# Optimization experiments

Hardware: AMD Instinct MI355X
Metric: run time of the kernel (lower is better)

The kernel has to match this reference:

```python
import jax, jax.numpy as jnp
import numpy as np
import math

B, T, S = 8, 8, 64
L = T * S            # 512 tokens per modality
D = 1024             # bi_hidden_size
H = 16               # bi_num_attention_heads
DH = D // H          # 64 head size (queries)
DKV = D // 2         # 512 kv projection size
SCALE = 1.0 / math.sqrt(DH)


def setup_inputs() -> dict:
    key = jax.random.key(0)
    ks = jax.random.split(key, 24)
    inp = {
        "input_tensor1": jax.random.normal(ks[0], (B, T, S, D), jnp.float32),
        "attention_mask1": jnp.zeros((B, 1, 1, L), jnp.float32),
        "input_tensor2": jax.random.normal(ks[1], (B, T, S, D), jnp.float32),
        "attention_mask2": jnp.zeros((B, 1, 1, L), jnp.float32),
        "input_tensor3": jax.random.normal(ks[2], (B, T, S, D), jnp.float32),
        "attention_mask3": jnp.zeros((B, 1, 1, L), jnp.float32),
    }
    # Linear params, stored as [in, out]; y = x @ W + b
    kidx = 3
    for i in (1, 2, 3):
        inp[f"w_q{i}"] = jax.random.normal(ks[kidx], (D, D), jnp.float32) * 0.02; kidx += 1
        inp[f"b_q{i}"] = jnp.zeros((D,), jnp.float32)
        inp[f"w_k{i}"] = jax.random.normal(ks[kidx], (D, DKV), jnp.float32) * 0.02; kidx += 1
        inp[f"b_k{i}"] = jnp.zeros((DKV,), jnp.float32)
        inp[f"w_v{i}"] = jax.random.normal(ks[kidx], (D, DKV), jnp.float32) * 0.02; kidx += 1
        inp[f"b_v{i}"] = jnp.zeros((DKV,), jnp.float32)
    return inp


def _heads(x):
    # [B, L, H*dh] -> [B, H, L, dh]
    b, l, d = x.shape
    return x.reshape(b, l, H, d // H).transpose(0, 2, 1, 3)


def _branch(q, k_a, k_b, v_a, v_b, bias):
    # keys/values concatenated along the per-head feature dim (dim 3)
    k = jnp.concatenate([k_a, k_b], axis=-1)          # [B,H,L,dh]
    v = jnp.concatenate([v_a, v_b], axis=-1)          # [B,H,L,dh]
    scores = jnp.einsum('bhqd,bhkd->bhqk', q, k) * SCALE + bias
    probs = jax.nn.softmax(scores, axis=-1)           # [B,H,L,L]
    ctx = jnp.einsum('bhqk,bhkd->bhqd', probs, v)     # [B,H,L,dh]
    ctx = ctx.transpose(0, 2, 1, 3).reshape(q.shape[0], T, S, D)
    return ctx, probs


def reference(input_tensor1, attention_mask1, input_tensor2, attention_mask2,
              input_tensor3, attention_mask3,
              w_q1, b_q1, w_k1, b_k1, w_v1, b_v1,
              w_q2, b_q2, w_k2, b_k2, w_v2, b_v2,
              w_q3, b_q3, w_k3, b_k3, w_v3, b_v3):
    b = input_tensor1.shape[0]
    x1 = input_tensor1.reshape(b, L, -1)
    x2 = input_tensor2.reshape(b, L, -1)
    x3 = input_tensor3.reshape(b, L, -1)
    m1 = attention_mask1.reshape(b, 1, 1, L)
    m2 = attention_mask2.reshape(b, 1, 1, L)
    m3 = attention_mask3.reshape(b, 1, 1, L)

    q1 = _heads(x1 @ w_q1 + b_q1); k1 = _heads(x1 @ w_k1 + b_k1); v1 = _heads(x1 @ w_v1 + b_v1)
    q2 = _heads(x2 @ w_q2 + b_q2); k2 = _heads(x2 @ w_k2 + b_k2); v2 = _heads(x2 @ w_v2 + b_v2)
    q3 = _heads(x3 @ w_q3 + b_q3); k3 = _heads(x3 @ w_k3 + b_k3); v3 = _heads(x3 @ w_v3 + b_v3)

    # branch 1: Q from modality2, KV from 1+3, mask bias from masks 1&3
    c1, p1 = _branch(q2, k1, k3, v1, v3, m1 + m3)
    # branch 2: Q from modality1, KV from 2+3, no mask bias
    c2, p2 = _branch(q1, k2, k3, v2, v3, jnp.zeros((), jnp.float32))
    # branch 3: Q from modality3, KV from 1+2, mask bias from masks 1&2
    c3, p3 = _branch(q3, k1, k2, v1, v2, m1 + m2)

    return (c2, c1, c3, (p2, p1, p3))
```

## Files before the change

### kernel.cpp

```cpp
#include <hip/hip_runtime.h>
#include <hip/hip_bf16.h>

typedef __bf16 bf16x8 __attribute__((ext_vector_type(8)));
typedef float f32x4 __attribute__((ext_vector_type(4)));

#define ATT_SCALE 0.125f

static __device__ __forceinline__ unsigned short f2bf(float f){
  unsigned u = __float_as_uint(f);
  u += 0x7fffu + ((u >> 16) & 1u);
  return (unsigned short)(u >> 16);
}
static __device__ __forceinline__ bf16x8 ld_bf8(const unsigned short* p){
  uint4 u = *(const uint4*)p;
  return __builtin_bit_cast(bf16x8, u);
}
static __device__ __forceinline__ f32x4 mfma16(bf16x8 a, bf16x8 b, f32x4 c){
  return __builtin_amdgcn_mfma_f32_16x16x32_bf16(a, b, c, 0, 0, 0);
}
static __device__ __forceinline__ void gload16(const unsigned short* g, unsigned short* l){
  __builtin_amdgcn_global_load_lds(
      (const __attribute__((address_space(1))) unsigned*)g,
      (__attribute__((address_space(3))) unsigned*)l, 16, 0, 0);
}
static __device__ __forceinline__ void lgkm_bar(){
  asm volatile("s_waitcnt lgkmcnt(0)" ::: "memory");
  __builtin_amdgcn_s_barrier();
  __builtin_amdgcn_sched_barrier(0);
}

struct WtArgs { const float* src[9]; unsigned short* dst[9]; int N[9]; };
__global__ void wtrans(WtArgs a){
  int z = blockIdx.z;
  int N = a.N[z];
  int n0 = blockIdx.x*32;
  if(n0 >= N) return;
  int k0 = blockIdx.y*32;
  const float* W = a.src[z];
  unsigned short* WT = a.dst[z];
  __shared__ float t[32][33];
  int tx = threadIdx.x, ty = threadIdx.y;
  #pragma unroll
  for(int r=0;r<4;++r){
    int row = ty + r*8;
    t[row][tx] = W[(size_t)(k0+row)*N + n0+tx];
  }
  __syncthreads();
  #pragma unroll
  for(int r=0;r<4;++r){
    int row = ty + r*8;
    WT[(size_t)(n0+row)*1024 + k0+tx] = f2bf(t[tx][row]);
  }
}

struct GemmArgs {
  const float* X[3]; const unsigned short* WT[3];
  const float* bq[3]; const float* bk[3]; const float* bv[3];
  unsigned short* C[3];
};
__global__ __launch_bounds__(256) void gemm_qkv(GemmArgs g){
  __shared__ unsigned short As[128*32];
  __shared__ unsigned short Bs[128*32];
  int z = blockIdx.z;
  const float* A = g.X[z];
  const unsigned short* Bt = g.WT[z];
  unsigned short* C = g.C[z];
  int tid = threadIdx.x;
  int wave = tid>>6, lane = tid&63, l15 = lane&15, l4 = lane>>4;
  int m0 = blockIdx.y*128, n0 = blockIdx.x*128;
  int wr = wave>>1, wc = wave&1;
  f32x4 acc[4][4];
  #pragma unroll
  for(int i=0;i<4;++i)
    #pragma unroll
    for(int j=0;j<4;++j) acc[i][j] = (f32x4){0.f,0.f,0.f,0.f};

  int c0r = tid,      row0 = c0r>>2, col0 = (c0r&3)*8;
  int c1r = tid+256,  row1 = c1r>>2, col1 = (c1r&3)*8;
  const float* a0p = A + (size_t)(m0+row0)*1024 + col0;
  const float* a1p = A + (size_t)(m0+row1)*1024 + col1;
  const unsigned short* b0p = Bt + (size_t)(n0+row0)*1024 + col0;
  const unsigned short* b1p = Bt + (size_t)(n0+row1)*1024 + col1;

  for(int k0=0; k0<1024; k0+=32){
    gload16(b0p + k0, &Bs[c0r*8]);
    gload16(b1p + k0, &Bs[c1r*8]);
    float4 fa0 = *(const float4*)(a0p + k0);
    float4 fa1 = *(const float4*)(a0p + k0 + 4);
    float4 fb0 = *(const float4*)(a1p + k0);
    float4 fb1 = *(const float4*)(a1p + k0 + 4);
    ushort4 u0 = {f2bf(fa0.x), f2bf(fa0.y), f2bf(fa0.z), f2bf(fa0.w)};
    ushort4 u1 = {f2bf(fa1.x), f2bf(fa1.y), f2bf(fa1.z), f2bf(fa1.w)};
    ushort4 u2 = {f2bf(fb0.x), f2bf(fb0.y), f2bf(fb0.z), f2bf(fb0.w)};
    ushort4 u3 = {f2bf(fb1.x), f2bf(fb1.y), f2bf(fb1.z), f2bf(fb1.w)};
    *(ushort4*)&As[c0r*8]     = u0;
    *(ushort4*)&As[c0r*8 + 4] = u1;
    *(ushort4*)&As[c1r*8]     = u2;
    *(ushort4*)&As[c1r*8 + 4] = u3;
    __syncthreads();
    bf16x8 af[4], bfr[4];
    #pragma unroll
    for(int t=0;t<4;++t){
      af[t]  = ld_bf8(&As[(wr*64 + t*16 + l15)*32 + 8*l4]);
      bfr[t] = ld_bf8(&Bs[(wc*64 + t*16 + l15)*32 + 8*l4]);
    }
    #pragma unroll
    for(int mt=0;mt<4;++mt)
      #pragma unroll
      for(int nt=0;nt<4;++nt)
        acc[mt][nt] = mfma16(af[mt], bfr[nt], acc[mt][nt]);
    __syncthreads();
  }

  #pragma unroll
  for(int mt=0;mt<4;++mt){
    #pragma unroll
    for(int nt=0;nt<4;++nt){
      int col = n0 + wc*64 + nt*16 + l15;
      float bb;
      if(col < 1024)      bb = g.bq[z][col];
      else if(col < 1536) bb = g.bk[z][col-1024];
      else                bb = g.bv[z][col-1536];
      #pragma unroll
      for(int r=0;r<4;++r){
        int row = m0 + wr*64 + mt*16 + l4*4 + r;
        C[(size_t)row*2048 + col] = f2bf(acc[mt][nt][r] + bb);
      }
    }
  }
}

struct VtArgs { const unsigned short* in[3]; unsigned short* out[3]; };
__global__ __launch_bounds__(256) void vtrans(VtArgs a){
  int z = blockIdx.z;
  const unsigned short* in = a.in[z];
  unsigned short* out = a.out[z];
  __shared__ unsigned short T[64][72];
  int r0 = blockIdx.x*64, c0 = blockIdx.y*64;
  int tid = threadIdx.x;
  #pragma unroll
  for(int p=0;p<4;++p){
    int e = p*1024 + tid*4;
    int row = e>>6, col = e&63;
    *(ushort4*)&T[row][col] = *(const ushort4*)&in[(size_t)(r0+row)*2048 + c0+col];
  }
  __syncthreads();
  #pragma unroll
  for(int p=0;p<4;++p){
    int e = p*1024 + tid*4;
    int orow = e>>6, ocol = e&63;
    ushort4 v = {T[ocol][orow], T[ocol+1][orow], T[ocol+2][orow], T[ocol+3][orow]};
    *(ushort4*)&out[(size_t)(c0+orow)*4096 + r0+ocol] = v;
  }
}

struct AttnArgs {
  const unsigned short* Q[3];  const unsigned short* Ka[3]; const unsigned short* Kb[3];
  const unsigned short* VTa[3]; const unsigned short* VTb[3];
  const float* mA[3]; const float* mB[3];
  float* ctx[3]; float* probs[3];
};
__global__ __launch_bounds__(256) void attn(AttnArgs A){
  __shared__ float S[16*512];
  int wg = blockIdx.x;
  int id = (wg & 7)*768 + (wg >> 3);
  int br = id >> 11;
  int rem = id & 2047;
  int bh = rem >> 4, pr = rem & 15;
  int b = bh >> 4, h = bh & 15;
  const unsigned short* Q   = A.Q[br];
  const unsigned short* Ka  = A.Ka[br];
  const unsigned short* Kb  = A.Kb[br];
  const unsigned short* VTa = A.VTa[br];
  const unsigned short* VTb = A.VTb[br];
  const float* mA = A.mA[br];
  const float* mB = A.mB[br];
  float* ctx   = A.ctx[br];
  float* probs = A.probs[br];

  int tid = threadIdx.x, wave = tid>>6, lane = tid&63, l15 = lane&15, l4 = lane>>4;
  int q0A = pr*32;

  f32x4 msk4[2] = {{0.f,0.f,0.f,0.f},{0.f,0.f,0.f,0.f}};
  #pragma unroll
  for(int it=0; it<2; ++it){
    int c = it*256 + lane*4;
    if(mA) msk4[it] += *(const f32x4*)&mA[b*512 + c];
    if(mB) msk4[it] += *(const f32x4*)&mB[b*512 + c];
  }

  const unsigned short* qp = Q + (size_t)(b*512 + q0A + l15)*2048 + h*64 + 8*l4;
  bf16x8 qa0 = ld_bf8(qp);
  bf16x8 qa1 = ld_bf8(qp + 32);
  bf16x8 qb0 = ld_bf8(qp + 16*2048);
  bf16x8 qb1 = ld_bf8(qp + 16*2048 + 32);

  int ct0 = wave*8;
  const unsigned short* kap = Ka + (size_t)(b*512 + ct0*16 + l15)*2048 + h*32 + 8*l4;
  const unsigned short* kbp = Kb + (size_t)(b*512 + ct0*16 + l15)*2048 + h*32 + 8*l4;
  bf16x8 ka[8], kb[8];
  #pragma unroll
  for(int t=0;t<8;++t){
    ka[t] = ld_bf8(kap + (size_t)t*16*2048);
    kb[t] = ld_bf8(kbp + (size_t)t*16*2048);
  }

  int d0 = wave*16 + l15;
  const unsigned short* vb0 = (d0<32 ? VTa + (size_t)(h*32+d0)*4096 : VTb + (size_t)(h*32+d0-32)*4096) + b*512;
  bf16x8 vpre[8];
  #pragma unroll
  for(int kc=0;kc<8;++kc) vpre[kc] = ld_bf8(vb0 + kc*32 + 8*l4);

  #pragma unroll
  for(int tile=0; tile<2; ++tile){
    int q0 = q0A + tile*16;
    bf16x8 a0 = tile ? qb0 : qa0;
    bf16x8 a1 = tile ? qb1 : qa1;
    if(tile) lgkm_bar();

    #pragma unroll
    for(int t=0;t<8;++t){
      int ct = ct0 + t;
      f32x4 acc = (f32x4){0.f,0.f,0.f,0.f};
      acc = mfma16(a0, ka[t], acc);
      acc = mfma16(a1, kb[t], acc);
      #pragma unroll
      for(int r=0;r<4;++r){
        int row = l4*4 + r;
        int col = ct*16 + l15;
        S[row*512 + ((((col>>2) ^ (row&7)) << 2) | (col&3))] = acc[r];
      }
    }
    lgkm_bar();

    for(int rr=0; rr<4; ++rr){
      int r = wave*4 + rr;
      float* rowp = &S[r*512];
      int x = r & 7;
      f32x4 v[2];
      float m = -1e30f;
      #pragma unroll
      for(int it=0; it<2; ++it){
        int c4 = it*64 + lane;
        v[it] = *(const f32x4*)&rowp[(c4 ^ x) << 2];
        v[it] = v[it]*ATT_SCALE + msk4[it];
        m = fmaxf(m, fmaxf(fmaxf(v[it][0], v[it][1]), fmaxf(v[it][2], v[it][3])));
      }
      #pragma unroll
      for(int o=32;o;o>>=1) m = fmaxf(m, __shfl_xor(m, o));
      float sum = 0.f;
      #pragma unroll
      for(int it=0; it<2; ++it){
        #pragma unroll
        for(int j=0;j<4;++j){
          v[it][j] = __expf(v[it][j]-m);
          sum += v[it][j];
        }
      }
      #pragma unroll
      for(int o=32;o;o>>=1) sum += __shfl_xor(sum, o);
      float inv = 1.0f/sum;
      float* po = probs + ((size_t)bh*512 + (q0+r))*512;
      #pragma unroll
      for(int it=0; it<2; ++it){
        int c4 = it*64 + lane;
        f32x4 p = v[it]*inv;
        *(f32x4*)&rowp[(c4 ^ x) << 2] = p;
        *(f32x4*)&po[it*256 + lane*4] = p;
      }
    }
    lgkm_bar();

    int px = l15 & 7;
    const float* prowp = &S[l15*512];
    f32x4 accE = (f32x4){0.f,0.f,0.f,0.f}, accO = (f32x4){0.f,0.f,0.f,0.f};
    #pragma unroll
    for(int kc=0;kc<16;++kc){
      int c4a = kc*8 + 2*l4;
      float4 v0 = *(const float4*)&prowp[(c4a ^ px) << 2];
      float4 v1 = *(const float4*)&prowp[((c4a+1) ^ px) << 2];
      bf16x8 a = { (__bf16)v0.x,(__bf16)v0.y,(__bf16)v0.z,(__bf16)v0.w,
                   (__bf16)v1.x,(__bf16)v1.y,(__bf16)v1.z,(__bf16)v1.w };
      bf16x8 bb = (kc < 8) ? vpre[kc] : ld_bf8(vb0 + kc*32 + 8*l4);
      if(kc & 1) accO = mfma16(a, bb, accO);
      else       accE = mfma16(a, bb, accE);
    }
    f32x4 acc = accE + accO;
    #pragma unroll
    for(int r=0;r<4;++r){
      int row = q0 + l4*4 + r;
      ctx[((size_t)(b*512+row))*1024 + h*64 + d0] = acc[r];
    }
  }
}

extern "C" void kernel_launch(void* const* d_in, const int* in_sizes, int n_in,
                              void* d_out, int out_size, void* d_ws, size_t ws_size,
                              hipStream_t stream){
  const float* x[3]    = {(const float*)d_in[0], (const float*)d_in[2], (const float*)d_in[4]};
  const float* mask[3] = {(const float*)d_in[1], (const float*)d_in[3], (const float*)d_in[5]};
  const float *wq[3], *bq[3], *wk[3], *bk[3], *wv[3], *bv[3];
  for(int i=0;i<3;++i){
    wq[i]=(const float*)d_in[6+6*i];  bq[i]=(const float*)d_in[7+6*i];
    wk[i]=(const float*)d_in[8+6*i];  bk[i]=(const float*)d_in[9+6*i];
    wv[i]=(const float*)d_in[10+6*i]; bv[i]=(const float*)d_in[11+6*i];
  }

  unsigned short* ws = (unsigned short*)d_ws;
  unsigned short *WT[3], *QKV[3], *VT[3];
  for(int i=0;i<3;++i){
    VT[i]  = ws + (size_t)i*4194304;
    WT[i]  = ws + 12582912 + (size_t)i*2097152;
    QKV[i] = ws + 18874368 + (size_t)i*8388608;
  }

  WtArgs wa;
  for(int i=0;i<3;++i){
    wa.src[3*i+0]=wq[i]; wa.dst[3*i+0]=WT[i];           wa.N[3*i+0]=1024;
    wa.src[3*i+1]=wk[i]; wa.dst[3*i+1]=WT[i]+1048576;   wa.N[3*i+1]=512;
    wa.src[3*i+2]=wv[i]; wa.dst[3*i+2]=WT[i]+1572864;   wa.N[3*i+2]=512;
  }
  wtrans<<<dim3(32,32,9), dim3(32,8), 0, stream>>>(wa);

  GemmArgs ga;
  for(int i=0;i<3;++i){
    ga.X[i]=x[i]; ga.WT[i]=WT[i]; ga.bq[i]=bq[i]; ga.bk[i]=bk[i]; ga.bv[i]=bv[i]; ga.C[i]=QKV[i];
  }
  gemm_qkv<<<dim3(16,32,3), 256, 0, stream>>>(ga);

  VtArgs va;
  for(int i=0;i<3;++i){ va.in[i]=QKV[i]+1536; va.out[i]=VT[i]; }
  vtrans<<<dim3(64,8,3), 256, 0, stream>>>(va);

  float* out = (float*)d_out;
  float* ctx2 = out;
  float* ctx1 = out + 4194304;
  float* ctx3 = out + 8388608;
  float* p2   = out + 12582912;
  float* p1   = out + 46137344;
  float* p3   = out + 79691776;

  AttnArgs aa;
  aa.Q[0]=QKV[0]; aa.Ka[0]=QKV[1]+1024; aa.Kb[0]=QKV[2]+1024; aa.VTa[0]=VT[1]; aa.VTb[0]=VT[2];
  aa.mA[0]=nullptr; aa.mB[0]=nullptr; aa.ctx[0]=ctx2; aa.probs[0]=p2;
  aa.Q[1]=QKV[1]; aa.Ka[1]=QKV[0]+1024; aa.Kb[1]=QKV[2]+1024; aa.VTa[1]=VT[0]; aa.VTb[1]=VT[2];
  aa.mA[1]=mask[0]; aa.mB[1]=mask[2]; aa.ctx[1]=ctx1; aa.probs[1]=p1;
  aa.Q[2]=QKV[2]; aa.Ka[2]=QKV[0]+1024; aa.Kb[2]=QKV[1]+1024; aa.VTa[2]=VT[0]; aa.VTb[2]=VT[1];
  aa.mA[2]=mask[0]; aa.mB[2]=mask[1]; aa.ctx[2]=ctx3; aa.probs[2]=p3;
  attn<<<6144, 256, 0, stream>>>(aa);
}
```

Baseline: 341.7 us.

## Split attention into 16-row blocks with parallel-row softmax and bf16 LDS probs

Each workgroup now handles one 16-query tile instead of two, which doubles the grid to 12288 blocks. Softmax is restructured so each wave processes 4 rows at once, with 16 lanes per row and 16-lane shuffle reductions, instead of looping serially over rows. Probabilities are written back to LDS as bf16 in a swizzled layout, so the PV MFMA loads operands directly without per-use float-to-bf16 conversion. The trade-off is that K and V fragments are now reloaded twice as often across blocks, raising global and L2 traffic.

```diff
diff --git a/kernel.cpp b/kernel.cpp
--- a/kernel.cpp
+++ b/kernel.cpp
@@ -163,10 +163,10 @@
 __global__ __launch_bounds__(256) void attn(AttnArgs A){
   __shared__ float S[16*512];
   int wg = blockIdx.x;
-  int id = (wg & 7)*768 + (wg >> 3);
-  int br = id >> 11;
-  int rem = id & 2047;
-  int bh = rem >> 4, pr = rem & 15;
+  int id = (wg & 7)*1536 + (wg >> 3);
+  int br = id >> 12;
+  int rem = id & 4095;
+  int bh = rem >> 5, qt = rem & 31;
   int b = bh >> 4, h = bh & 15;
   const unsigned short* Q   = A.Q[br];
   const unsigned short* Ka  = A.Ka[br];
@@ -179,21 +179,21 @@
   float* probs = A.probs[br];
 
   int tid = threadIdx.x, wave = tid>>6, lane = tid&63, l15 = lane&15, l4 = lane>>4;
-  int q0A = pr*32;
-
-  f32x4 msk4[2] = {{0.f,0.f,0.f,0.f},{0.f,0.f,0.f,0.f}};
-  #pragma unroll
-  for(int it=0; it<2; ++it){
-    int c = it*256 + lane*4;
-    if(mA) msk4[it] += *(const f32x4*)&mA[b*512 + c];
-    if(mB) msk4[it] += *(const f32x4*)&mB[b*512 + c];
-  }
-
-  const unsigned short* qp = Q + (size_t)(b*512 + q0A + l15)*2048 + h*64 + 8*l4;
-  bf16x8 qa0 = ld_bf8(qp);
-  bf16x8 qa1 = ld_bf8(qp + 32);
-  bf16x8 qb0 = ld_bf8(qp + 16*2048);
-  bf16x8 qb1 = ld_bf8(qp + 16*2048 + 32);
+  int q0 = qt*16;
+
+  f32x4 msk[8];
+  #pragma unroll
+  for(int j=0;j<8;++j){
+    f32x4 v = (f32x4){0.f,0.f,0.f,0.f};
+    int c = b*512 + (l15 + j*16)*4;
+    if(mA) v += *(const f32x4*)&mA[c];
+    if(mB) v += *(const f32x4*)&mB[c];
+    msk[j] = v;
+  }
+
+  const unsigned short* qp = Q + (size_t)(b*512 + q0 + l15)*2048 + h*64 + 8*l4;
+  bf16x8 a0 = ld_bf8(qp);
+  bf16x8 a1 = ld_bf8(qp + 32);
 
   int ct0 = wave*8;
   const unsigned short* kap = Ka + (size_t)(b*512 + ct0*16 + l15)*2048 + h*32 + 8*l4;
@@ -212,75 +212,68 @@
   for(int kc=0;kc<8;++kc) vpre[kc] = ld_bf8(vb0 + kc*32 + 8*l4);
 
   #pragma unroll
-  for(int tile=0; tile<2; ++tile){
-    int q0 = q0A + tile*16;
-    bf16x8 a0 = tile ? qb0 : qa0;
-    bf16x8 a1 = tile ? qb1 : qa1;
-    if(tile) lgkm_bar();
-
-    #pragma unroll
-    for(int t=0;t<8;++t){
-      int ct = ct0 + t;
-      f32x4 acc = (f32x4){0.f,0.f,0.f,0.f};
-      acc = mfma16(a0, ka[t], acc);
-      acc = mfma16(a1, kb[t], acc);
+  for(int t=0;t<8;++t){
+    int ct = ct0 + t;
+    f32x4 acc = (f32x4){0.f,0.f,0.f,0.f};
+    acc = mfma16(a0, ka[t], acc);
+    acc = mfma16(a1, kb[t], acc);
+    #pragma unroll
+    for(int r=0;r<4;++r){
+      int row = l4*4 + r;
+      int col = ct*16 + l15;
+      S[row*512 + ((((col>>2) ^ (row&7)) << 2) | (col&3))] = acc[r];
+    }
+  }
+  lgkm_bar();
+
+  {
+    int r = wave*4 + l4;
+    int x = r & 7;
+    float* rowp = &S[r*512];
+    unsigned short* Pl = (unsigned short*)S;
+    f32x4 v[8];
+    float m = -1e30f;
+    #pragma unroll
+    for(int j=0;j<8;++j){
+      int lu = l15 + j*16;
+      v[j] = *(const f32x4*)&rowp[(lu ^ x) << 2];
+      v[j] = v[j]*ATT_SCALE + msk[j];
+      m = fmaxf(m, fmaxf(fmaxf(v[j][0], v[j][1]), fmaxf(v[j][2], v[j][3])));
+    }
+    #pragma unroll
+    for(int o=1;o<16;o<<=1) m = fmaxf(m, __shfl_xor(m, o));
+    float sum = 0.f;
+    #pragma unroll
+    for(int j=0;j<8;++j){
       #pragma unroll
-      for(int r=0;r<4;++r){
-        int row = l4*4 + r;
-        int col = ct*16 + l15;
-        S[row*512 + ((((col>>2) ^ (row&7)) << 2) | (col&3))] = acc[r];
+      for(int w=0;w<4;++w){
+        v[j][w] = __expf(v[j][w] - m);
+        sum += v[j][w];
       }
     }
-    lgkm_bar();
-
-    for(int rr=0; rr<4; ++rr){
-      int r = wave*4 + rr;
-      float* rowp = &S[r*512];
-      int x = r & 7;
-      f32x4 v[2];
-      float m = -1e30f;
-      #pragma unroll
-      for(int it=0; it<2; ++it){
-        int c4 = it*64 + lane;
-        v[it] = *(const f32x4*)&rowp[(c4 ^ x) << 2];
-        v[it] = v[it]*ATT_SCALE + msk4[it];
-        m = fmaxf(m, fmaxf(fmaxf(v[it][0], v[it][1]), fmaxf(v[it][2], v[it][3])));
-      }
-      #pragma unroll
-      for(int o=32;o;o>>=1) m = fmaxf(m, __shfl_xor(m, o));
-      float sum = 0.f;
-      #pragma unroll
-      for(int it=0; it<2; ++it){
-        #pragma unroll
-        for(int j=0;j<4;++j){
-          v[it][j] = __expf(v[it][j]-m);
-          sum += v[it][j];
-        }
-      }
-      #pragma unroll
-      for(int o=32;o;o>>=1) sum += __shfl_xor(sum, o);
-      float inv = 1.0f/sum;
-      float* po = probs + ((size_t)bh*512 + (q0+r))*512;
-      #pragma unroll
-      for(int it=0; it<2; ++it){
-        int c4 = it*64 + lane;
-        f32x4 p = v[it]*inv;
-        *(f32x4*)&rowp[(c4 ^ x) << 2] = p;
-        *(f32x4*)&po[it*256 + lane*4] = p;
-      }
-    }
-    lgkm_bar();
-
-    int px = l15 & 7;
-    const float* prowp = &S[l15*512];
+    #pragma unroll
+    for(int o=1;o<16;o<<=1) sum += __shfl_xor(sum, o);
+    float inv = 1.0f/sum;
+    float* po = probs + ((size_t)bh*512 + (q0+r))*512;
+    #pragma unroll
+    for(int j=0;j<8;++j){
+      int lu = l15 + j*16;
+      f32x4 p = v[j]*inv;
+      *(f32x4*)&po[lu*4] = p;
+      ushort4 pb = {f2bf(p[0]), f2bf(p[1]), f2bf(p[2]), f2bf(p[3])};
+      *(ushort4*)&Pl[r*1024 + (((lu>>1) ^ x) << 3) + (lu&1)*4] = pb;
+    }
+  }
+  lgkm_bar();
+
+  {
+    const unsigned short* prow = (const unsigned short*)S + l15*1024;
+    int xr = l15 & 7;
     f32x4 accE = (f32x4){0.f,0.f,0.f,0.f}, accO = (f32x4){0.f,0.f,0.f,0.f};
     #pragma unroll
     for(int kc=0;kc<16;++kc){
-      int c4a = kc*8 + 2*l4;
-      float4 v0 = *(const float4*)&prowp[(c4a ^ px) << 2];
-      float4 v1 = *(const float4*)&prowp[((c4a+1) ^ px) << 2];
-      bf16x8 a = { (__bf16)v0.x,(__bf16)v0.y,(__bf16)v0.z,(__bf16)v0.w,
-                   (__bf16)v1.x,(__bf16)v1.y,(__bf16)v1.z,(__bf16)v1.w };
+      int u = kc*4 + l4;
+      bf16x8 a = ld_bf8(prow + ((u ^ xr) << 3));
       bf16x8 bb = (kc < 8) ? vpre[kc] : ld_bf8(vb0 + kc*32 + 8*l4);
       if(kc & 1) accO = mfma16(a, bb, accO);
       else       accE = mfma16(a, bb, accE);
@@ -347,5 +340,5 @@
   aa.mA[1]=mask[0]; aa.mB[1]=mask[2]; aa.ctx[1]=ctx1; aa.probs[1]=p1;
   aa.Q[2]=QKV[2]; aa.Ka[2]=QKV[0]+1024; aa.Kb[2]=QKV[1]+1024; aa.VTa[2]=VT[0]; aa.VTb[2]=VT[1];
   aa.mA[2]=mask[0]; aa.mB[2]=mask[1]; aa.ctx[2]=ctx3; aa.probs[2]=p3;
-  attn<<<6144, 256, 0, stream>>>(aa);
-}
+  attn<<<12288, 256, 0, stream>>>(aa);
+}
```

Result: slower. 413.5 us (+21.0%).
